# Kernel optimization log

Hardware: AMD Instinct MI355X
Metric: run time of the kernel (lower is better)

## Reference

```python
import jax, jax.numpy as jnp
import numpy as np

B, S, D_MODEL, H = 2, 2048, 1024, 16
HD = D_MODEL // H  # 64
THETA = 10000.0


def setup_inputs() -> dict:
    key = jax.random.key(0)
    ks = jax.random.split(key, 5)
    std = (2.0 / (D_MODEL + D_MODEL)) ** 0.5
    x = jax.random.normal(ks[0], (B, S, D_MODEL), dtype=jnp.float32)
    Wq = jax.random.normal(ks[1], (D_MODEL, D_MODEL), dtype=jnp.float32) * std
    Wk = jax.random.normal(ks[2], (D_MODEL, D_MODEL), dtype=jnp.float32) * std
    Wv = jax.random.normal(ks[3], (D_MODEL, D_MODEL), dtype=jnp.float32) * std
    Wo = jax.random.normal(ks[4], (D_MODEL, D_MODEL), dtype=jnp.float32) * std
    # RoPE tables (buffers)
    pos = jnp.arange(S, dtype=jnp.float32)
    freq = THETA ** (-jnp.arange(0, HD, 2, dtype=jnp.float32) / HD)  # [HD/2]
    ang = jnp.outer(pos, freq)  # [S, HD/2]
    token_positions = jnp.arange(S, dtype=jnp.int32)
    return {
        "x": x,
        "token_positions": token_positions,
        "use_rope": 1,
        "Wq": Wq, "Wk": Wk, "Wv": Wv, "Wo": Wo,
        "cos": jnp.cos(ang), "sin": jnp.sin(ang),
    }


def _apply_rope(t, c, sn):
    # t: [b,h,s,d]; c,sn: [s,d/2] (broadcast over b,h)
    e = t[..., 0::2]
    o = t[..., 1::2]
    return jnp.stack([e * c - o * sn, o * c + e * sn], axis=-1).reshape(t.shape)


def reference(x, token_positions, use_rope, Wq, Wk, Wv, Wo, cos, sin):
    b, s, _ = x.shape

    def split_heads(t):  # [b,s,D] -> [b,h,s,hd]
        return t.reshape(b, s, H, HD).transpose(0, 2, 1, 3)

    q = split_heads(x @ Wq.T)
    k = split_heads(x @ Wk.T)
    v = split_heads(x @ Wv.T)

    if use_rope:
        c = cos[token_positions]   # [s, hd/2]
        sn = sin[token_positions]  # [s, hd/2]
        q = _apply_rope(q, c, sn)
        k = _apply_rope(k, c, sn)

    scale = 1.0 / jnp.sqrt(jnp.float32(HD))
    scores = jnp.einsum('bhqd,bhkd->bhqk', q, k) * scale  # [b,h,s,s]
    causal = jnp.tril(jnp.ones((s, s), dtype=bool))
    scores = jnp.where(causal, scores, -jnp.inf)
    attn = jax.nn.softmax(scores, axis=-1)
    y = jnp.einsum('bhqk,bhkd->bhqd', attn, v)
    y = y.transpose(0, 2, 1, 3).reshape(b, s, D_MODEL)
    return y @ Wo.T
```

## Files before the change

kernel.cpp:

```cpp
#include <hip/hip_runtime.h>
#include <math.h>

#define BB 2
#define SS 2048
#define DM 1024
#define NH 16
#define HD 64

typedef __attribute__((ext_vector_type(8))) __bf16 bf16x8;
typedef __attribute__((ext_vector_type(4))) __bf16 bf16x4;
typedef __attribute__((ext_vector_type(8))) unsigned short u16x8;
typedef __attribute__((ext_vector_type(4))) float f32x4;
typedef unsigned short u16;
typedef unsigned int u32;
typedef __attribute__((address_space(1))) unsigned int u32g;
typedef __attribute__((address_space(3))) unsigned int u32l;

#define CEXP 0.18033688011112042f

static __device__ __forceinline__ u16 f2bf(float f) {
    __bf16 h = (__bf16)f;
    return __builtin_bit_cast(unsigned short, h);
}

static __device__ __forceinline__ void gld16(const u16* g, u16* l) {
    __builtin_amdgcn_global_load_lds((const u32g*)g, (u32l*)l, 16, 0, 0);
}

__global__ __launch_bounds__(256)
void cast_all(const float* __restrict__ x,
              const float* __restrict__ wq, const float* __restrict__ wk,
              const float* __restrict__ wv, const float* __restrict__ wo,
              u16* __restrict__ xb, u16* __restrict__ wqb, u16* __restrict__ wkb,
              u16* __restrict__ wvb, u16* __restrict__ wob)
{
    const int N4X = (BB * SS * DM) / 4;
    const int N4W = (DM * DM) / 4;
    int i = blockIdx.x * 256 + threadIdx.x;
    const float* src; u16* dst; int off;
    if (i < N4X) { src = x; dst = xb; off = i; }
    else {
        int i2 = i - N4X;
        int w = i2 >> 18;
        off = i2 & (N4W - 1);
        switch (w) {
            case 0:  src = wq; dst = wqb; break;
            case 1:  src = wk; dst = wkb; break;
            case 2:  src = wv; dst = wvb; break;
            default: src = wo; dst = wob; break;
        }
    }
    float4 v = ((const float4*)src)[off];
    ushort4 o;
    o.x = f2bf(v.x); o.y = f2bf(v.y); o.z = f2bf(v.z); o.w = f2bf(v.w);
    ((ushort4*)dst)[off] = o;
}

__global__ __launch_bounds__(256, 3)
void qkv_gemm(const u16* __restrict__ X,
              const u16* __restrict__ Wq, const u16* __restrict__ Wk,
              const u16* __restrict__ Wv,
              const int* __restrict__ tp, const float* __restrict__ cosp,
              const float* __restrict__ sinp, const int* __restrict__ use_rope,
              u16* __restrict__ Q, u16* __restrict__ K, u16* __restrict__ V)
{
    const u16* W; u16* dst;
    if (blockIdx.z == 0)      { W = Wq; dst = Q; }
    else if (blockIdx.z == 1) { W = Wk; dst = K; }
    else                      { W = Wv; dst = V; }

    __shared__ u16 SH[4 * 64 * 68];
    u16* As = SH;
    u16* Bs = SH + 8192;
    const int t  = threadIdx.x;
    const int wv = t >> 6, L = t & 63, ln = L & 15, qd = L >> 4;
    const int i0 = blockIdx.y * 128, j0 = blockIdx.x * 128;
    const int wm = (wv >> 1) * 64, wn = (wv & 1) * 64;
    const int srow = L >> 3;
    const int scg  = ((L & 7) ^ (L >> 3)) * 8;

    f32x4 acc[4][4];
    #pragma unroll
    for (int a = 0; a < 4; ++a)
        #pragma unroll
        for (int b = 0; b < 4; ++b)
            #pragma unroll
            for (int e = 0; e < 4; ++e) acc[a][b][e] = 0.f;

    for (int k0 = 0; k0 < DM; k0 += 64) {
        __syncthreads();
        #pragma unroll
        for (int g = 0; g < 4; ++g) {
            int rb = wv * 32 + g * 8;
            gld16(X + (size_t)(i0 + rb + srow) * DM + k0 + scg, &As[rb * 64]);
            gld16(W + (size_t)(j0 + rb + srow) * DM + k0 + scg, &Bs[rb * 64]);
        }
        __syncthreads();
        bf16x8 a[4][2], b[4][2];
        #pragma unroll
        for (int mi = 0; mi < 4; ++mi)
            #pragma unroll
            for (int kd = 0; kd < 2; ++kd)
                a[mi][kd] = *(const bf16x8*)&As[(wm + mi * 16 + ln) * 64 + (((kd * 4 + qd) ^ (ln & 7)) * 8)];
        #pragma unroll
        for (int ni = 0; ni < 4; ++ni)
            #pragma unroll
            for (int kd = 0; kd < 2; ++kd)
                b[ni][kd] = *(const bf16x8*)&Bs[(wn + ni * 16 + ln) * 64 + (((kd * 4 + qd) ^ (ln & 7)) * 8)];
        #pragma unroll
        for (int kd = 0; kd < 2; ++kd)
            #pragma unroll
            for (int mi = 0; mi < 4; ++mi)
                #pragma unroll
                for (int ni = 0; ni < 4; ++ni)
                    acc[mi][ni] = __builtin_amdgcn_mfma_f32_16x16x32_bf16(a[mi][kd], b[ni][kd], acc[mi][ni], 0, 0, 0);
    }

    const int rope_on = (blockIdx.z < 2) ? use_rope[0] : 0;
    if (rope_on) {
        #pragma unroll
        for (int mi = 0; mi < 4; ++mi)
            #pragma unroll
            for (int r = 0; r < 4; ++r) {
                int gi = i0 + wm + mi * 16 + qd * 4 + r;
                int s = gi & 2047;
                int pos = tp[s];
                #pragma unroll
                for (int ni = 0; ni < 4; ++ni) {
                    int d = wn + ni * 16 + ln;
                    int dh = d & 63;
                    float c  = cosp[pos * 32 + (dh >> 1)];
                    float sn = sinp[pos * 32 + (dh >> 1)];
                    float v = acc[mi][ni][r];
                    float pv = __shfl_xor(v, 1);
                    acc[mi][ni][r] = (dh & 1) ? (v * c + pv * sn) : (v * c - pv * sn);
                }
            }
    }

    __syncthreads();
    u16* Ts = SH + wv * (64 * 68);
    #pragma unroll
    for (int mi = 0; mi < 4; ++mi)
        #pragma unroll
        for (int ni = 0; ni < 4; ++ni)
            #pragma unroll
            for (int r = 0; r < 4; ++r)
                Ts[(mi * 16 + qd * 4 + r) * 68 + ni * 16 + ln] = f2bf(acc[mi][ni][r]);

    const int h  = blockIdx.x * 2 + (wv & 1);
    const int sb = i0 + wm;
    const int b_ = sb >> 11, s0 = sb & 2047;
    if (blockIdx.z < 2) {
        const int lrow = L >> 3, lcol = (L & 7) * 8;
        #pragma unroll
        for (int r2 = 0; r2 < 8; ++r2) {
            int row = lrow + r2 * 8;
            u16x8 val = *(const u16x8*)&Ts[row * 68 + lcol];
            *(u16x8*)&dst[(((size_t)(b_ * NH + h)) * SS + s0 + row) * HD + lcol] = val;
        }
    } else {
        const int sch = (L & 7) * 8;
        const int dr0 = L >> 3;
        #pragma unroll
        for (int r2 = 0; r2 < 8; ++r2) {
            int d = dr0 + r2 * 8;
            u16x8 val;
            #pragma unroll
            for (int u = 0; u < 8; ++u) val[u] = Ts[(sch + u) * 68 + d];
            *(u16x8*)&dst[(((size_t)(b_ * NH + h)) * HD + d) * SS + s0 + sch] = val;
        }
    }
}

__global__ __launch_bounds__(256, 2)
void out_gemm(const u16* __restrict__ X, const u16* __restrict__ W,
              float* __restrict__ dst)
{
    __shared__ char SHB[36864];
    u16* As = (u16*)SHB;
    u16* Bs = (u16*)SHB + 8192;
    const int t  = threadIdx.x;
    const int wv = t >> 6, L = t & 63, ln = L & 15, qd = L >> 4;
    const int i0 = blockIdx.y * 128, j0 = blockIdx.x * 64;
    const int wm = (wv >> 1) * 64, wn = (wv & 1) * 32;
    const int srow = L >> 3;
    const int scg  = ((L & 7) ^ (L >> 3)) * 8;

    f32x4 acc[4][2];
    #pragma unroll
    for (int mi = 0; mi < 4; ++mi)
        #pragma unroll
        for (int ni = 0; ni < 2; ++ni)
            #pragma unroll
            for (int e = 0; e < 4; ++e) acc[mi][ni][e] = 0.f;

    for (int k0 = 0; k0 < DM; k0 += 64) {
        __syncthreads();
        #pragma unroll
        for (int g = 0; g < 4; ++g) {
            int rb = wv * 32 + g * 8;
            gld16(X + (size_t)(i0 + rb + srow) * DM + k0 + scg, &As[rb * 64]);
        }
        #pragma unroll
        for (int g = 0; g < 2; ++g) {
            int rb = wv * 16 + g * 8;
            gld16(W + (size_t)(j0 + rb + srow) * DM + k0 + scg, &Bs[rb * 64]);
        }
        __syncthreads();
        bf16x8 a[4][2], b[2][2];
        #pragma unroll
        for (int mi = 0; mi < 4; ++mi)
            #pragma unroll
            for (int kd = 0; kd < 2; ++kd)
                a[mi][kd] = *(const bf16x8*)&As[(wm + mi * 16 + ln) * 64 + (((kd * 4 + qd) ^ (ln & 7)) * 8)];
        #pragma unroll
        for (int ni = 0; ni < 2; ++ni)
            #pragma unroll
            for (int kd = 0; kd < 2; ++kd)
                b[ni][kd] = *(const bf16x8*)&Bs[(wn + ni * 16 + ln) * 64 + (((kd * 4 + qd) ^ (ln & 7)) * 8)];
        #pragma unroll
        for (int kd = 0; kd < 2; ++kd)
            #pragma unroll
            for (int mi = 0; mi < 4; ++mi)
                #pragma unroll
                for (int ni = 0; ni < 2; ++ni)
                    acc[mi][ni] = __builtin_amdgcn_mfma_f32_16x16x32_bf16(a[mi][kd], b[ni][kd], acc[mi][ni], 0, 0, 0);
    }

    __syncthreads();
    float* Ts = (float*)SHB + wv * (64 * 36);
    #pragma unroll
    for (int mi = 0; mi < 4; ++mi)
        #pragma unroll
        for (int ni = 0; ni < 2; ++ni)
            #pragma unroll
            for (int r = 0; r < 4; ++r)
                Ts[(mi * 16 + qd * 4 + r) * 36 + ni * 16 + ln] = acc[mi][ni][r];

    const int lrow = L >> 3, lch = L & 7;
    #pragma unroll
    for (int r2 = 0; r2 < 8; ++r2) {
        int row = lrow + r2 * 8;
        float4 v = *(const float4*)&Ts[row * 36 + lch * 4];
        *(float4*)&dst[(size_t)(i0 + wm + row) * DM + j0 + wn + lch * 4] = v;
    }
}

static __device__ __forceinline__ void group_step(
    const u16* KsB, const bf16x8 qf[2], u16* psw,
    bool diag, int rowg, int j0, int ln, int qd,
    float& m, float& l, f32x4* o, bf16x8& pf0, bf16x8& pf1)
{
    const int pm = 2 * (ln & 7);
    f32x4 s[4];
    #pragma unroll
    for (int mt = 0; mt < 4; ++mt) {
        bf16x8 a0 = *(const bf16x8*)&KsB[(mt * 16 + ln) * 64 + ((qd ^ (ln & 7)) * 8)];
        bf16x8 a1 = *(const bf16x8*)&KsB[(mt * 16 + ln) * 64 + (((4 + qd) ^ (ln & 7)) * 8)];
        #pragma unroll
        for (int e = 0; e < 4; ++e) s[mt][e] = 0.f;
        s[mt] = __builtin_amdgcn_mfma_f32_16x16x32_bf16(a0, qf[0], s[mt], 0, 0, 0);
        s[mt] = __builtin_amdgcn_mfma_f32_16x16x32_bf16(a1, qf[1], s[mt], 0, 0, 0);
    }
    if (diag) {
        #pragma unroll
        for (int mt = 0; mt < 4; ++mt)
            #pragma unroll
            for (int r = 0; r < 4; ++r)
                if (j0 + mt * 16 + qd * 4 + r > rowg) s[mt][r] = -3.0e38f;
    }
    float rm = s[0][0];
    #pragma unroll
    for (int mt = 0; mt < 4; ++mt)
        #pragma unroll
        for (int r = 0; r < 4; ++r) rm = fmaxf(rm, s[mt][r]);
    rm = fmaxf(rm, __shfl_xor(rm, 16));
    rm = fmaxf(rm, __shfl_xor(rm, 32));
    float nm = fmaxf(m, rm);
    float alpha = exp2f((m - nm) * CEXP);
    float nmc = nm * CEXP;
    float rs = 0.f;
    #pragma unroll
    for (int mt = 0; mt < 4; ++mt) {
        bf16x4 pk;
        #pragma unroll
        for (int r = 0; r < 4; ++r) {
            float pv = exp2f(fmaf(s[mt][r], CEXP, -nmc));
            rs += pv;
            pk[r] = (__bf16)pv;
        }
        *(bf16x4*)(psw + ln * 64 + ((mt * 4 + qd) ^ pm) * 4) = pk;
    }
    rs += __shfl_xor(rs, 16);
    rs += __shfl_xor(rs, 32);
    l = l * alpha + rs;
    m = nm;
    #pragma unroll
    for (int ni = 0; ni < 4; ++ni)
        #pragma unroll
        for (int r = 0; r < 4; ++r) o[ni][r] *= alpha;
    pf0 = *(const bf16x8*)(psw + ln * 64 + ((qd * 2) ^ pm) * 4);
    pf1 = *(const bf16x8*)(psw + ln * 64 + ((8 + qd * 2) ^ pm) * 4);
}

__global__ __launch_bounds__(512, 4)
void attn_kernel(const u16* __restrict__ Q, const u16* __restrict__ K,
                 const u16* __restrict__ V, u16* __restrict__ Y)
{
    __shared__ u16 Ks[2][64 * 64];
    __shared__ u16 Vt[2][64 * 64];
    __shared__ u16 Ps[8][16 * 64];

    const int t  = threadIdx.x;
    const int wv = t >> 6, L = t & 63, ln = L & 15, qd = L >> 4;
    const int wsub = wv & 3, grp = wv >> 2;
    const int bh = blockIdx.x, p = blockIdx.y;
    const int qb = (grp ? (31 - p) : p) * 64;
    const u16* Qp = Q + (size_t)bh * SS * HD;
    const u16* Kp = K + (size_t)bh * SS * HD;
    const u16* Vp = V + (size_t)bh * HD * SS;
    const int srow = L >> 3;
    const int scg  = ((L & 7) ^ (L >> 3)) * 8;

    const int ntile   = 32 - p;
    const int myTiles = grp ? ntile : (p + 1);

    bf16x8 qf[2];
    {
        const u16* rq = Qp + (size_t)(qb + wsub * 16 + ln) * HD;
        qf[0] = *(const bf16x8*)(rq + qd * 8);
        qf[1] = *(const bf16x8*)(rq + 32 + qd * 8);
    }

    f32x4 o[4];
    #pragma unroll
    for (int ni = 0; ni < 4; ++ni)
        #pragma unroll
        for (int e = 0; e < 4; ++e) o[ni][e] = 0.f;
    float m = -3.0e38f, l = 0.f;

    gld16(Kp + (size_t)(wv * 8 + srow) * HD + scg, &Ks[0][(wv * 8) * 64]);
    gld16(Vp + (size_t)(wv * 8 + srow) * SS + scg, &Vt[0][(wv * 8) * 64]);
    __syncthreads();

    for (int tix = 0; tix < ntile; ++tix) {
        const int j0 = tix * 64;
        const int buf = tix & 1;
        const bool more = (tix + 1 < ntile);

        if (more) {
            const int j1 = j0 + 64;
            gld16(Kp + (size_t)(j1 + wv * 8 + srow) * HD + scg, &Ks[buf ^ 1][(wv * 8) * 64]);
            gld16(Vp + (size_t)(wv * 8 + srow) * SS + j1 + scg, &Vt[buf ^ 1][(wv * 8) * 64]);
        }

        if (tix < myTiles) {
            bf16x8 pf0, pf1;
            group_step(Ks[buf], qf, &Ps[wv][0], tix == myTiles - 1,
                       qb + wsub * 16 + ln, j0, ln, qd, m, l, o, pf0, pf1);
            #pragma unroll
            for (int kc = 0; kc < 2; ++kc)
                #pragma unroll
                for (int ni = 0; ni < 4; ++ni) {
                    bf16x8 vf = *(const bf16x8*)&Vt[buf][(ni * 16 + ln) * 64 + (((kc * 4 + qd) ^ (ln & 7)) * 8)];
                    o[ni] = __builtin_amdgcn_mfma_f32_16x16x32_bf16(vf, kc ? pf1 : pf0, o[ni], 0, 0, 0);
                }
        }
        __syncthreads();
    }

    const int b = bh >> 4, h = bh & 15;
    const float inv = 1.f / l;
    const int sq = qb + wsub * 16 + ln;
    #pragma unroll
    for (int ni = 0; ni < 4; ++ni) {
        bf16x4 pk;
        #pragma unroll
        for (int r = 0; r < 4; ++r) pk[r] = (__bf16)(o[ni][r] * inv);
        *(bf16x4*)&Y[((size_t)(b * SS + sq)) * DM + h * HD + ni * 16 + qd * 4] = pk;
    }
}

extern "C" void kernel_launch(void* const* d_in, const int* in_sizes, int n_in,
                              void* d_out, int out_size, void* d_ws, size_t ws_size,
                              hipStream_t stream)
{
    const float* x        = (const float*)d_in[0];
    const int*   tp       = (const int*)d_in[1];
    const int*   use_rope = (const int*)d_in[2];
    const float* Wq       = (const float*)d_in[3];
    const float* Wk       = (const float*)d_in[4];
    const float* Wv       = (const float*)d_in[5];
    const float* Wo       = (const float*)d_in[6];
    const float* cosp     = (const float*)d_in[7];
    const float* sinp     = (const float*)d_in[8];
    float* out = (float*)d_out;

    char* ws = (char*)d_ws;
    const size_t MB = 1 << 20;
    u16* xb  = (u16*)(ws);
    u16* Wqb = (u16*)(ws + 8 * MB);
    u16* Wkb = (u16*)(ws + 10 * MB);
    u16* Wvb = (u16*)(ws + 12 * MB);
    u16* Wob = (u16*)(ws + 14 * MB);
    u16* Qb  = (u16*)(ws + 16 * MB);
    u16* Kb  = (u16*)(ws + 24 * MB);
    u16* Vb  = (u16*)(ws + 32 * MB);
    u16* Yb  = (u16*)(ws + 40 * MB);

    cast_all<<<8192, 256, 0, stream>>>(x, Wq, Wk, Wv, Wo, xb, Wqb, Wkb, Wvb, Wob);
    qkv_gemm<<<dim3(DM / 128, BB * SS / 128, 3), 256, 0, stream>>>(
        xb, Wqb, Wkb, Wvb, tp, cosp, sinp, use_rope, Qb, Kb, Vb);
    attn_kernel<<<dim3(BB * NH, 16), 512, 0, stream>>>(Qb, Kb, Vb, Yb);
    out_gemm<<<dim3(DM / 64, BB * SS / 128), 256, 0, stream>>>(Yb, Wob, out);
}
```

Before: 185.8 us.

## Split each query tile's KV range across two wave groups with LSE merge

Each block now handles its two query tiles (p and 31-p) one after another instead of at the same time. For each tile, the two four-wave groups take disjoint halves of the key/value tiles, each with its own double-buffered K/V shared memory, and the partial softmax states (m, l, o) are merged through shared memory before the output is written. This is meant to balance the work of the two groups and to lower register pressure, since only one query tile is live per wave. The cost is twice the K/V LDS footprint, launch bounds cut from 4 to 2 blocks, extra barriers, and a serial two-phase structure.

```diff
diff --git a/kernel.cpp b/kernel.cpp
--- a/kernel.cpp
+++ b/kernel.cpp
@@ -304,81 +304,121 @@
     pf1 = *(const bf16x8*)(psw + ln * 64 + ((8 + qd * 2) ^ pm) * 4);
 }
 
-__global__ __launch_bounds__(512, 4)
+__global__ __launch_bounds__(512, 2)
 void attn_kernel(const u16* __restrict__ Q, const u16* __restrict__ K,
                  const u16* __restrict__ V, u16* __restrict__ Y)
 {
-    __shared__ u16 Ks[2][64 * 64];
-    __shared__ u16 Vt[2][64 * 64];
+    __shared__ u16 Ks[2][2][64 * 64];
+    __shared__ u16 Vt[2][2][64 * 64];
     __shared__ u16 Ps[8][16 * 64];
 
     const int t  = threadIdx.x;
     const int wv = t >> 6, L = t & 63, ln = L & 15, qd = L >> 4;
-    const int wsub = wv & 3, grp = wv >> 2;
+    const int grp = wv >> 2, wsub = wv & 3;
     const int bh = blockIdx.x, p = blockIdx.y;
-    const int qb = (grp ? (31 - p) : p) * 64;
     const u16* Qp = Q + (size_t)bh * SS * HD;
     const u16* Kp = K + (size_t)bh * SS * HD;
     const u16* Vp = V + (size_t)bh * HD * SS;
     const int srow = L >> 3;
     const int scg  = ((L & 7) ^ (L >> 3)) * 8;
-
-    const int ntile   = 32 - p;
-    const int myTiles = grp ? ntile : (p + 1);
-
-    bf16x8 qf[2];
-    {
-        const u16* rq = Qp + (size_t)(qb + wsub * 16 + ln) * HD;
-        qf[0] = *(const bf16x8*)(rq + qd * 8);
-        qf[1] = *(const bf16x8*)(rq + 32 + qd * 8);
-    }
-
-    f32x4 o[4];
-    #pragma unroll
-    for (int ni = 0; ni < 4; ++ni)
-        #pragma unroll
-        for (int e = 0; e < 4; ++e) o[ni][e] = 0.f;
-    float m = -3.0e38f, l = 0.f;
-
-    gld16(Kp + (size_t)(wv * 8 + srow) * HD + scg, &Ks[0][(wv * 8) * 64]);
-    gld16(Vp + (size_t)(wv * 8 + srow) * SS + scg, &Vt[0][(wv * 8) * 64]);
-    __syncthreads();
-
-    for (int tix = 0; tix < ntile; ++tix) {
-        const int j0 = tix * 64;
-        const int buf = tix & 1;
-        const bool more = (tix + 1 < ntile);
-
-        if (more) {
-            const int j1 = j0 + 64;
-            gld16(Kp + (size_t)(j1 + wv * 8 + srow) * HD + scg, &Ks[buf ^ 1][(wv * 8) * 64]);
-            gld16(Vp + (size_t)(wv * 8 + srow) * SS + j1 + scg, &Vt[buf ^ 1][(wv * 8) * 64]);
-        }
-
-        if (tix < myTiles) {
-            bf16x8 pf0, pf1;
-            group_step(Ks[buf], qf, &Ps[wv][0], tix == myTiles - 1,
-                       qb + wsub * 16 + ln, j0, ln, qd, m, l, o, pf0, pf1);
-            #pragma unroll
-            for (int kc = 0; kc < 2; ++kc)
-                #pragma unroll
-                for (int ni = 0; ni < 4; ++ni) {
-                    bf16x8 vf = *(const bf16x8*)&Vt[buf][(ni * 16 + ln) * 64 + (((kc * 4 + qd) ^ (ln & 7)) * 8)];
-                    o[ni] = __builtin_amdgcn_mfma_f32_16x16x32_bf16(vf, kc ? pf1 : pf0, o[ni], 0, 0, 0);
+    const int b = bh >> 4, h = bh & 15;
+
+    float* MB = (float*)&Ks[1][0][0];
+    float* ML = (float*)&Ps[4][0];
+
+    #pragma unroll 1
+    for (int ph = 0; ph < 2; ++ph) {
+        const int qt    = ph ? (31 - p) : p;
+        const int qb    = qt * 64;
+        const int ntile = qt + 1;
+        const int half0 = ntile >> 1;
+        const int I     = ntile - half0;
+        const int base  = grp ? half0 : 0;
+        const int cnt   = grp ? I : half0;
+
+        bf16x8 qf[2];
+        {
+            const u16* rq = Qp + (size_t)(qb + wsub * 16 + ln) * HD;
+            qf[0] = *(const bf16x8*)(rq + qd * 8);
+            qf[1] = *(const bf16x8*)(rq + 32 + qd * 8);
+        }
+
+        f32x4 o[4];
+        #pragma unroll
+        for (int ni = 0; ni < 4; ++ni)
+            #pragma unroll
+            for (int e = 0; e < 4; ++e) o[ni][e] = 0.f;
+        float m = -3.0e38f, l = 0.f;
+
+        if (cnt > 0) {
+            #pragma unroll
+            for (int g = 0; g < 2; ++g) {
+                int rb = wsub * 16 + g * 8;
+                gld16(Kp + (size_t)(base * 64 + rb + srow) * HD + scg, &Ks[grp][0][rb * 64]);
+                gld16(Vp + (size_t)(rb + srow) * SS + base * 64 + scg, &Vt[grp][0][rb * 64]);
+            }
+        }
+        __syncthreads();
+
+        #pragma unroll 1
+        for (int tix = 0; tix < I; ++tix) {
+            const int buf = tix & 1;
+
+            if (tix + 1 < cnt) {
+                const int j1 = (base + tix + 1) * 64;
+                #pragma unroll
+                for (int g = 0; g < 2; ++g) {
+                    int rb = wsub * 16 + g * 8;
+                    gld16(Kp + (size_t)(j1 + rb + srow) * HD + scg, &Ks[grp][buf ^ 1][rb * 64]);
+                    gld16(Vp + (size_t)(rb + srow) * SS + j1 + scg, &Vt[grp][buf ^ 1][rb * 64]);
                 }
-        }
-        __syncthreads();
-    }
-
-    const int b = bh >> 4, h = bh & 15;
-    const float inv = 1.f / l;
-    const int sq = qb + wsub * 16 + ln;
-    #pragma unroll
-    for (int ni = 0; ni < 4; ++ni) {
-        bf16x4 pk;
-        #pragma unroll
-        for (int r = 0; r < 4; ++r) pk[r] = (__bf16)(o[ni][r] * inv);
-        *(bf16x4*)&Y[((size_t)(b * SS + sq)) * DM + h * HD + ni * 16 + qd * 4] = pk;
+            }
+
+            if (tix < cnt) {
+                const int gt = base + tix;
+                bf16x8 pf0, pf1;
+                group_step(&Ks[grp][buf][0], qf, &Ps[wv][0],
+                           grp && (tix == cnt - 1),
+                           qb + wsub * 16 + ln, gt * 64, ln, qd, m, l, o, pf0, pf1);
+                #pragma unroll
+                for (int kc = 0; kc < 2; ++kc)
+                    #pragma unroll
+                    for (int ni = 0; ni < 4; ++ni) {
+                        bf16x8 vf = *(const bf16x8*)&Vt[grp][buf][(ni * 16 + ln) * 64 + (((kc * 4 + qd) ^ (ln & 7)) * 8)];
+                        o[ni] = __builtin_amdgcn_mfma_f32_16x16x32_bf16(vf, kc ? pf1 : pf0, o[ni], 0, 0, 0);
+                    }
+            }
+            __syncthreads();
+        }
+
+        const int writer = ph ? 0 : 1;
+        const int q = wsub * 16 + ln;
+        if (grp == writer) {
+            if (qd == 0) { ML[q] = m; ML[64 + q] = l; }
+            #pragma unroll
+            for (int ni = 0; ni < 4; ++ni)
+                *(f32x4*)&MB[q * 64 + ni * 16 + qd * 4] = o[ni];
+        }
+        __syncthreads();
+        if (grp != writer) {
+            float mp = ML[q], lp = ML[64 + q];
+            float mf = fmaxf(m, mp);
+            float as = exp2f((m - mf) * CEXP);
+            float ap = exp2f((mp - mf) * CEXP);
+            float lf = as * l + ap * lp;
+            float inv = 1.f / lf;
+            const int sq = qb + q;
+            #pragma unroll
+            for (int ni = 0; ni < 4; ++ni) {
+                f32x4 op = *(const f32x4*)&MB[q * 64 + ni * 16 + qd * 4];
+                bf16x4 pk;
+                #pragma unroll
+                for (int r = 0; r < 4; ++r)
+                    pk[r] = (__bf16)((as * o[ni][r] + ap * op[r]) * inv);
+                *(bf16x4*)&Y[((size_t)(b * SS + sq)) * DM + h * HD + ni * 16 + qd * 4] = pk;
+            }
+        }
+        __syncthreads();
     }
 }
 
```

After: 186.6 us. No clear change (+0.5%).
